# Optimization experiments

Hardware: AMD Instinct MI355X
Metric: run time of the kernel (lower is better)

Reference implementation:

```python
import jax, jax.numpy as jnp
import numpy as np

N, E, B = 100000, 1600000, 128
F_E, F_X, F_U, H = 128, 128, 128, 64
F_U_OUT = 128


def setup_inputs() -> dict:
    key = jax.random.key(0)
    ks = jax.random.split(key, 16)
    s = lambda fan_in: 1.0 / np.sqrt(fan_in)
    inp = {
        "x": jax.random.normal(ks[0], (N, F_X), jnp.float32),
        "e": jax.random.normal(ks[1], (E, F_E), jnp.float32),
        "u": jax.random.normal(ks[2], (B, F_U), jnp.float32),
        "edge_index": jax.random.randint(ks[3], (2, E), 0, N, jnp.int64),
        "batch": jnp.sort(jax.random.randint(ks[4], (N,), 0, B, jnp.int64)),
        # attention projection params
        "Wk_e": jax.random.uniform(ks[5], (F_E, H), jnp.float32, -s(F_E), s(F_E)),
        "bk_e": jnp.zeros((H,), jnp.float32),
        "Wq_e": jax.random.uniform(ks[6], (F_U, H), jnp.float32, -s(F_U), s(F_U)),
        "bq_e": jnp.zeros((H,), jnp.float32),
        "Wk_x": jax.random.uniform(ks[7], (F_X, H), jnp.float32, -s(F_X), s(F_X)),
        "bk_x": jnp.zeros((H,), jnp.float32),
        "Wq_x": jax.random.uniform(ks[8], (F_U, H), jnp.float32, -s(F_U), s(F_U)),
        "bq_x": jnp.zeros((H,), jnp.float32),
        # phi_u (model_fn = single Linear)
        "Wu": jax.random.uniform(ks[9], (F_E + F_X + F_U, F_U_OUT), jnp.float32,
                                  -s(F_E + F_X + F_U), s(F_E + F_X + F_U)),
        "bu": jnp.zeros((F_U_OUT,), jnp.float32),
    }
    return inp


def reference(x, e, u, edge_index, batch,
              Wk_e, bk_e, Wq_e, bq_e, Wk_x, bk_x, Wq_x, bq_x, Wu, bu):
    num_graphs = u.shape[0]
    src = edge_index[0]
    e_batch = batch[src]                       # [E] graph id per edge

    # edge attention: sigmoid(<k_e, q_e>) per edge, then scatter-add per graph
    k = e @ Wk_e + bk_e                        # [E, H]
    q = (u @ Wq_e + bq_e)[e_batch]             # [E, H] gather
    a_e = jax.nn.sigmoid(jnp.sum(k * q, axis=-1, keepdims=True))  # [E, 1]
    e_agg = jax.ops.segment_sum(a_e * e, e_batch, num_segments=num_graphs)  # [B, F_E]

    # node attention
    kx = x @ Wk_x + bk_x                       # [N, H]
    qx = (u @ Wq_x + bq_x)[batch]              # [N, H] gather
    a_x = jax.nn.sigmoid(jnp.sum(kx * qx, axis=-1, keepdims=True))  # [N, 1]
    x_agg = jax.ops.segment_sum(a_x * x, batch, num_segments=num_graphs)  # [B, F_X]

    out = jnp.concatenate([x_agg, e_agg, u], axis=1)  # [B, F_X+F_E+F_U]
    return out @ Wu + bu                        # [B, F_U_OUT]
```

## Files before the change

kernel.cpp:

```cpp
#include <hip/hip_runtime.h>
#include <hip/hip_bf16.h>


#define FDIM 128
#define BGRAPH 128
#define HDIM 64
#define SLICES 16
#define CAP 16384
#define CURSOR_STRIDE 16
#define SC_THREADS 512
#define SC_ITEMS 16
#define SC_TOTAL (SC_THREADS * SC_ITEMS)
#define MAXCHUNK (CAP / SLICES)

typedef float vf4 __attribute__((ext_vector_type(4)));

__device__ inline vf4 ldnt4(const float* p) {
    return __builtin_nontemporal_load(reinterpret_cast<const vf4*>(p));
}

__global__ __launch_bounds__(SC_THREADS) void prep_kernel(
    const int* __restrict__ src, const int* __restrict__ batch,
    int* __restrict__ cursor,
    int* __restrict__ order,
    float* __restrict__ x_agg,
    const float* __restrict__ x,
    const float* __restrict__ u,
    const float* __restrict__ Wk_e, const float* __restrict__ bk_e,
    const float* __restrict__ Wq_e, const float* __restrict__ bq_e,
    const float* __restrict__ Wk_x, const float* __restrict__ bk_x,
    const float* __restrict__ Wq_x, const float* __restrict__ bq_x,
    float* __restrict__ v_e, float* __restrict__ c_e,
    int E, int N, int nb_edge)
{
    const int t = threadIdx.x;

    if (blockIdx.x < nb_edge) {
        __shared__ int lh[BGRAPH];
        __shared__ int s_lofs[BGRAPH];
        __shared__ int s_gbase[BGRAPH];
        __shared__ int wtot[2];
        __shared__ int s_ids[SC_TOTAL];
        __shared__ unsigned char s_bin[SC_TOTAL];

        if (t < BGRAPH) lh[t] = 0;
        __syncthreads();

        const int base0 = blockIdx.x * SC_TOTAL;
        const int nval_blk = min(SC_TOTAL, E - base0);

        int iv[SC_ITEMS];
#pragma unroll
        for (int k = 0; k < SC_ITEMS; ++k) {
            const int i = base0 + k * SC_THREADS + t;
            iv[k] = (i < E) ? __builtin_nontemporal_load(src + i) : -1;
        }
        int gv[SC_ITEMS];
#pragma unroll
        for (int k = 0; k < SC_ITEMS; ++k)
            gv[k] = (iv[k] >= 0) ? batch[iv[k]] : -1;
        int rv[SC_ITEMS];
#pragma unroll
        for (int k = 0; k < SC_ITEMS; ++k)
            rv[k] = (gv[k] >= 0) ? atomicAdd(&lh[gv[k]], 1) : 0;
        __syncthreads();

        if (t < BGRAPH) {
            const int val = lh[t];
            int xs = val;
            for (int off = 1; off < 64; off <<= 1) {
                const int y = __shfl_up(xs, off, 64);
                if ((t & 63) >= off) xs += y;
            }
            if ((t & 63) == 63) wtot[t >> 6] = xs;
            s_lofs[t] = xs - val;
        }
        __syncthreads();
        if (t < BGRAPH) {
            const int lofs = s_lofs[t] + ((t >= 64) ? wtot[0] : 0);
            s_lofs[t] = lofs;
            const int n = lh[t];
            const int gb = (n > 0) ? atomicAdd(&cursor[t * CURSOR_STRIDE], n) : 0;
            s_gbase[t] = t * CAP + gb - lofs;
        }
        __syncthreads();

#pragma unroll
        for (int k = 0; k < SC_ITEMS; ++k) {
            if (gv[k] >= 0) {
                const int slot = s_lofs[gv[k]] + rv[k];
                s_ids[slot] = base0 + k * SC_THREADS + t;
                s_bin[slot] = (unsigned char)gv[k];
            }
        }
        __syncthreads();

        for (int p = t; p < nval_blk; p += SC_THREADS) {
            const int b = s_bin[p];
            order[s_gbase[b] + p] = s_ids[p];
        }
    } else {
        const int g2  = blockIdx.x - nb_edge;
        const int g   = g2 >> 1;
        const int par = g2 & 1;
        __shared__ float su[FDIM];
        __shared__ float sqe[HDIM];
        __shared__ float sqx[HDIM];
        __shared__ float s_vx[FDIM];
        __shared__ float s_cx;

        if (t < FDIM) su[t] = u[g * FDIM + t];
        __syncthreads();

        if (t < HDIM) {
            float acc = bq_e[t];
            for (int f = 0; f < FDIM; ++f) acc += su[f] * Wq_e[f * HDIM + t];
            sqe[t] = acc;
        } else if (t < 2 * HDIM) {
            const int h = t - HDIM;
            float acc = bq_x[h];
            for (int f = 0; f < FDIM; ++f) acc += su[f] * Wq_x[f * HDIM + h];
            sqx[h] = acc;
        }
        __syncthreads();

        if (t < FDIM) {
            float acce = 0.f, accx = 0.f;
            for (int h = 0; h < HDIM; ++h) {
                acce += Wk_e[t * HDIM + h] * sqe[h];
                accx += Wk_x[t * HDIM + h] * sqx[h];
            }
            if (par == 0) v_e[g * FDIM + t] = acce;
            s_vx[t] = accx;
        }
        if (t == 0) {
            float cx = 0.f;
            for (int h = 0; h < HDIM; ++h) cx += bk_x[h] * sqx[h];
            s_cx = cx;
            if (par == 0) {
                float ce = 0.f;
                for (int h = 0; h < HDIM; ++h) ce += bk_e[h] * sqe[h];
                c_e[g] = ce;
            }
        }
        __syncthreads();

        int lo = 0, hi = N;
        while (lo < hi) { int mid = (lo + hi) >> 1; if (batch[mid] < g) lo = mid + 1; else hi = mid; }
        const int start = lo;
        hi = N;
        while (lo < hi) { int mid = (lo + hi) >> 1; if (batch[mid] < g + 1) lo = mid + 1; else hi = mid; }
        const int end = lo;

        const int hidx = t >> 5;
        const int hl   = t & 31;
        const vf4 fv = *reinterpret_cast<const vf4*>(&s_vx[4 * hl]);
        const float cg = s_cx;

        vf4 acc = (vf4)(0.f);
        int row = start + 2 * hidx + par;
        vf4 fe = (vf4)(0.f);
        if (row < end) fe = ldnt4(x + (size_t)row * FDIM + 4 * hl);
        for (; row < end; row += 32) {
            vf4 fen = (vf4)(0.f);
            if (row + 32 < end) fen = ldnt4(x + (size_t)(row + 32) * FDIM + 4 * hl);
            float d = fe.x * fv.x + fe.y * fv.y + fe.z * fv.z + fe.w * fv.w;
            d += __shfl_xor(d, 1);
            d += __shfl_xor(d, 2);
            d += __shfl_xor(d, 4);
            d += __shfl_xor(d, 8);
            d += __shfl_xor(d, 16);
            const float a = 1.f / (1.f + __expf(-(d + cg)));
            acc.x += a * fe.x; acc.y += a * fe.y; acc.z += a * fe.z; acc.w += a * fe.w;
            fe = fen;
        }

        __shared__ float s_red[16][FDIM];
        s_red[hidx][4 * hl + 0] = acc.x;
        s_red[hidx][4 * hl + 1] = acc.y;
        s_red[hidx][4 * hl + 2] = acc.z;
        s_red[hidx][4 * hl + 3] = acc.w;
        __syncthreads();

        if (t < FDIM) {
            float ssum = 0.f;
#pragma unroll
            for (int k = 0; k < 16; ++k) ssum += s_red[k][t];
            unsafeAtomicAdd(&x_agg[g * FDIM + t], ssum);
        }
    }
}

__global__ __launch_bounds__(1024, 8) void agg_kernel(
    const float* __restrict__ e,
    const int*   __restrict__ order,
    const int*   __restrict__ cursor,
    const float* __restrict__ v_e, const float* __restrict__ c_e,
    float* __restrict__ e_agg)
{
    const int tid  = threadIdx.x;
    const int hidx = tid >> 5;
    const int hl   = tid & 31;
    __shared__ float s_red[32][FDIM];
    __shared__ int s_ids[MAXCHUNK];

    const int g = blockIdx.x / SLICES;
    const int s = blockIdx.x % SLICES;
    const int len = cursor[g * CURSOR_STRIDE];
    const int chunk = (len + SLICES - 1) / SLICES;
    const int clo = s * chunk;
    const int cnt = min(chunk, len - clo);

    for (int i = tid; i < cnt; i += 1024) s_ids[i] = order[g * CAP + clo + i];
    __syncthreads();

    const vf4 fv = *reinterpret_cast<const vf4*>(v_e + g * FDIM + 4 * hl);
    const float cg = c_e[g];

    vf4 acc = (vf4)(0.f);

    int p = hidx;
    vf4 f0 = (vf4)(0.f), f1 = (vf4)(0.f), f2 = (vf4)(0.f);
    if (p < cnt)      f0 = ldnt4(e + (size_t)s_ids[p]      * FDIM + 4 * hl);
    if (p + 32 < cnt) f1 = ldnt4(e + (size_t)s_ids[p + 32] * FDIM + 4 * hl);
    if (p + 64 < cnt) f2 = ldnt4(e + (size_t)s_ids[p + 64] * FDIM + 4 * hl);

    for (; p < cnt; p += 32) {
        vf4 f3 = (vf4)(0.f);
        if (p + 96 < cnt) f3 = ldnt4(e + (size_t)s_ids[p + 96] * FDIM + 4 * hl);

        float d = f0.x * fv.x + f0.y * fv.y + f0.z * fv.z + f0.w * fv.w;
        d += __shfl_xor(d, 1);
        d += __shfl_xor(d, 2);
        d += __shfl_xor(d, 4);
        d += __shfl_xor(d, 8);
        d += __shfl_xor(d, 16);
        const float a = 1.f / (1.f + __expf(-(d + cg)));
        acc.x += a * f0.x; acc.y += a * f0.y; acc.z += a * f0.z; acc.w += a * f0.w;

        f0 = f1; f1 = f2; f2 = f3;
    }

    s_red[hidx][4 * hl + 0] = acc.x;
    s_red[hidx][4 * hl + 1] = acc.y;
    s_red[hidx][4 * hl + 2] = acc.z;
    s_red[hidx][4 * hl + 3] = acc.w;
    __syncthreads();

    if (tid < FDIM) {
        float ssum = 0.f;
#pragma unroll
        for (int k = 0; k < 32; ++k) ssum += s_red[k][tid];
        unsafeAtomicAdd(&e_agg[g * FDIM + tid], ssum);
    }
}

__global__ __launch_bounds__(128) void final_kernel(
    const float* __restrict__ x_agg, const float* __restrict__ e_agg,
    const float* __restrict__ u,
    const float* __restrict__ Wu, const float* __restrict__ bu,
    float* __restrict__ out)
{
    const int g = blockIdx.x;
    const int o = threadIdx.x;
    __shared__ float cat[3 * FDIM];
    cat[o]            = x_agg[g * FDIM + o];
    cat[FDIM + o]     = e_agg[g * FDIM + o];
    cat[2 * FDIM + o] = u[g * FDIM + o];
    __syncthreads();

    float acc = bu[o];
#pragma unroll 8
    for (int r = 0; r < 3 * FDIM; ++r) acc += cat[r] * Wu[r * FDIM + o];
    out[g * FDIM + o] = acc;
}

extern "C" void kernel_launch(void* const* d_in, const int* in_sizes, int n_in,
                              void* d_out, int out_size, void* d_ws, size_t ws_size,
                              hipStream_t stream) {
    const float* x          = (const float*)d_in[0];
    const float* e          = (const float*)d_in[1];
    const float* u          = (const float*)d_in[2];
    const int*   edge_index = (const int*)d_in[3];
    const int*   batch      = (const int*)d_in[4];
    const float* Wk_e = (const float*)d_in[5];
    const float* bk_e = (const float*)d_in[6];
    const float* Wq_e = (const float*)d_in[7];
    const float* bq_e = (const float*)d_in[8];
    const float* Wk_x = (const float*)d_in[9];
    const float* bk_x = (const float*)d_in[10];
    const float* Wq_x = (const float*)d_in[11];
    const float* bq_x = (const float*)d_in[12];
    const float* Wu   = (const float*)d_in[13];
    const float* bu   = (const float*)d_in[14];

    const int N = in_sizes[4];
    const int E = in_sizes[3] / 2;
    const int* src = edge_index;

    float* ws    = (float*)d_ws;
    float* v_e   = ws;
    float* c_e   = v_e + BGRAPH * FDIM;
    float* e_agg = c_e + BGRAPH;
    float* x_agg = e_agg + BGRAPH * FDIM;
    int*   cursor = (int*)(x_agg + BGRAPH * FDIM);
    int*   order  = cursor + BGRAPH * CURSOR_STRIDE;

    hipMemsetAsync(e_agg, 0,
        (2 * BGRAPH * FDIM + BGRAPH * CURSOR_STRIDE) * sizeof(float), stream);

    const int nb_edge = (E + SC_TOTAL - 1) / SC_TOTAL;
    prep_kernel<<<nb_edge + 2 * BGRAPH, SC_THREADS, 0, stream>>>(
        src, batch, cursor, order, x_agg, x,
        u, Wk_e, bk_e, Wq_e, bq_e, Wk_x, bk_x, Wq_x, bq_x,
        v_e, c_e, E, N, nb_edge);

    agg_kernel<<<BGRAPH * SLICES, 1024, 0, stream>>>(
        e, order, cursor, v_e, c_e, e_agg);

    final_kernel<<<BGRAPH, 128, 0, stream>>>(
        x_agg, e_agg, u, Wu, bu, (float*)d_out);
}
```

Baseline: 197.3 us.

## Fuse final linear into agg kernel via last-block-done counter; double slices

Removes the separate final_kernel launch by having the last slice block per graph, detected through an atomic done counter, compute the output linear layer. It also doubles the number of slices per graph to spread edge aggregation across more blocks. The change trades one kernel launch for extra fences and atomics in every block, plus more atomic adds into e_agg.

```diff
diff --git a/kernel.cpp b/kernel.cpp
--- a/kernel.cpp
+++ b/kernel.cpp
@@ -5,7 +5,7 @@
 #define FDIM 128
 #define BGRAPH 128
 #define HDIM 64
-#define SLICES 16
+#define SLICES 32
 #define CAP 16384
 #define CURSOR_STRIDE 16
 #define SC_THREADS 512
@@ -196,13 +196,19 @@
     const int*   __restrict__ order,
     const int*   __restrict__ cursor,
     const float* __restrict__ v_e, const float* __restrict__ c_e,
-    float* __restrict__ e_agg)
+    float* __restrict__ e_agg,
+    int* __restrict__ done,
+    const float* __restrict__ x_agg,
+    const float* __restrict__ u,
+    const float* __restrict__ Wu, const float* __restrict__ bu,
+    float* __restrict__ out)
 {
     const int tid  = threadIdx.x;
     const int hidx = tid >> 5;
     const int hl   = tid & 31;
     __shared__ float s_red[32][FDIM];
     __shared__ int s_ids[MAXCHUNK];
+    __shared__ int s_win;
 
     const int g = blockIdx.x / SLICES;
     const int s = blockIdx.x % SLICES;
@@ -252,27 +258,34 @@
 #pragma unroll
         for (int k = 0; k < 32; ++k) ssum += s_red[k][tid];
         unsafeAtomicAdd(&e_agg[g * FDIM + tid], ssum);
-    }
-}
-
-__global__ __launch_bounds__(128) void final_kernel(
-    const float* __restrict__ x_agg, const float* __restrict__ e_agg,
-    const float* __restrict__ u,
-    const float* __restrict__ Wu, const float* __restrict__ bu,
-    float* __restrict__ out)
-{
-    const int g = blockIdx.x;
-    const int o = threadIdx.x;
-    __shared__ float cat[3 * FDIM];
-    cat[o]            = x_agg[g * FDIM + o];
-    cat[FDIM + o]     = e_agg[g * FDIM + o];
-    cat[2 * FDIM + o] = u[g * FDIM + o];
+        __threadfence();
+    }
     __syncthreads();
 
-    float acc = bu[o];
+    if (tid == 0) {
+        const int old = atomicAdd(&done[g], 1);
+        s_win = (old == SLICES - 1) ? 1 : 0;
+    }
+    __syncthreads();
+
+    if (s_win) {
+        __shared__ float cat[3 * FDIM];
+        if (tid < FDIM) {
+            __threadfence();
+            cat[FDIM + tid] = __hip_atomic_load(&e_agg[g * FDIM + tid],
+                                                __ATOMIC_RELAXED,
+                                                __HIP_MEMORY_SCOPE_AGENT);
+            cat[tid]            = x_agg[g * FDIM + tid];
+            cat[2 * FDIM + tid] = u[g * FDIM + tid];
+        }
+        __syncthreads();
+        if (tid < FDIM) {
+            float acc2 = bu[tid];
 #pragma unroll 8
-    for (int r = 0; r < 3 * FDIM; ++r) acc += cat[r] * Wu[r * FDIM + o];
-    out[g * FDIM + o] = acc;
+            for (int r = 0; r < 3 * FDIM; ++r) acc2 += cat[r] * Wu[r * FDIM + tid];
+            out[g * FDIM + tid] = acc2;
+        }
+    }
 }
 
 extern "C" void kernel_launch(void* const* d_in, const int* in_sizes, int n_in,
@@ -304,10 +317,12 @@
     float* e_agg = c_e + BGRAPH;
     float* x_agg = e_agg + BGRAPH * FDIM;
     int*   cursor = (int*)(x_agg + BGRAPH * FDIM);
-    int*   order  = cursor + BGRAPH * CURSOR_STRIDE;
+    int*   done   = cursor + BGRAPH * CURSOR_STRIDE;
+    int*   order  = done + BGRAPH;
 
     hipMemsetAsync(e_agg, 0,
-        (2 * BGRAPH * FDIM + BGRAPH * CURSOR_STRIDE) * sizeof(float), stream);
+        (2 * BGRAPH * FDIM + BGRAPH * CURSOR_STRIDE + BGRAPH) * sizeof(float),
+        stream);
 
     const int nb_edge = (E + SC_TOTAL - 1) / SC_TOTAL;
     prep_kernel<<<nb_edge + 2 * BGRAPH, SC_THREADS, 0, stream>>>(
@@ -316,8 +331,6 @@
         v_e, c_e, E, N, nb_edge);
 
     agg_kernel<<<BGRAPH * SLICES, 1024, 0, stream>>>(
-        e, order, cursor, v_e, c_e, e_agg);
-
-    final_kernel<<<BGRAPH, 128, 0, stream>>>(
-        x_agg, e_agg, u, Wu, bu, (float*)d_out);
+        e, order, cursor, v_e, c_e, e_agg, done, x_agg, u, Wu, bu,
+        (float*)d_out);
 }
```

Measured after the change: 659.2 us. 234% more time.
